# Kernel optimization log

Hardware: AMD Instinct MI355X
Metric: run time of the kernel (lower is better)

## Reference

```python
import jax, jax.numpy as jnp
import numpy as np

B, S, D, H, C = 8, 4096, 1024, 256, 512
INIT_RANGE = 0.01

def setup_inputs() -> dict:
    key = jax.random.key(0)
    ks = jax.random.split(key, 6)
    return {
        "hidden_states": jax.random.normal(ks[0], (B, S, D), dtype=jnp.float32),
        "conditions": jax.random.normal(ks[1], (B, C), dtype=jnp.float32),
        "down_project": jax.random.normal(ks[2], (D, H), dtype=jnp.float32) * INIT_RANGE,
        "down_gamma": jax.random.normal(ks[3], (C, H), dtype=jnp.float32),
        "down_beta": jnp.zeros((C, H), dtype=jnp.float32),
        "up_project": jax.random.normal(ks[4], (H, D), dtype=jnp.float32) * INIT_RANGE,
        "up_gamma": jax.random.normal(ks[5], (C, D), dtype=jnp.float32),
        "up_beta": jnp.zeros((C, D), dtype=jnp.float32),
    }

def reference(hidden_states, conditions, down_project, down_gamma, down_beta,
              up_project, up_gamma, up_beta):
    # per-example modulation coefficients: [B, H] / [B, D]
    dg = conditions @ down_gamma   # [B, H]
    db = conditions @ down_beta    # [B, H]
    ug = conditions @ up_gamma     # [B, D]
    ub = conditions @ up_beta      # [B, D]
    # per-example down weight: W_down * gamma (column scale) + beta (added to every row)
    w_down = down_project[None, :, :] * dg[:, None, :] + db[:, None, :]  # [B, D, H]
    down = jnp.einsum('bsd,bdh->bsh', hidden_states, w_down)             # [B, S, H]
    act = jax.nn.relu(down)
    w_up = up_project[None, :, :] * ug[:, None, :] + ub[:, None, :]      # [B, H, D]
    up = jnp.einsum('bsh,bhd->bsd', act, w_up)                           # [B, S, D]
    # (the original computes self.ln(up) but discards the result)
    return up + hidden_states
```

## Files before the change

kernel.cpp:

```cpp
#include <hip/hip_runtime.h>
#include <hip/hip_bf16.h>

typedef __attribute__((ext_vector_type(4))) float f32x4;
typedef __attribute__((ext_vector_type(8))) short s16x8;
typedef __attribute__((ext_vector_type(8))) unsigned short u16x8;
typedef __attribute__((ext_vector_type(4))) unsigned int u32x4;

#define DEVFN static __device__ __forceinline__

DEVFN unsigned short f2bf(float f) {
  union { float f; unsigned int u; } v; v.f = f;
  unsigned int u = v.u;
  u += 0x7fffu + ((u >> 16) & 1u);
  return (unsigned short)(u >> 16);
}

DEVFN unsigned int cvt_pk(float a, float b) {
  __hip_bfloat162 h = __float22bfloat162_rn(make_float2(a, b));
  union { __hip_bfloat162 h; unsigned int u; } v; v.h = h; return v.u;
}

DEVFN void gl_lds16(const void* g, void* l) {
  __builtin_amdgcn_global_load_lds((__attribute__((address_space(1))) void*)g,
                                   (__attribute__((address_space(3))) void*)l, 16, 0, 0);
}

#define DG_OFF 0
#define DB_OFF 2048
#define UG_OFF 4096
#define UB_OFF 12288
#define W1_BYTE 81920
#define W2_BYTE 606208

__global__ void prep_kernel(const float* __restrict__ cond,
                            const float* __restrict__ dgm, const float* __restrict__ dbt,
                            const float* __restrict__ ugm, const float* __restrict__ ubt,
                            const float* __restrict__ Wd, const float* __restrict__ Wu,
                            char* __restrict__ ws) {
  __shared__ float lc[4096];
  __shared__ float red[2048];
  const int t = threadIdx.x;

  if (blockIdx.x < 64) {
    const int bid = blockIdx.x;
    const float* src; char* dst; int C, ntile, kc;
    if (bid < 32) { src = Wd; C = 256;  ntile = bid >> 4; kc = bid & 15;
                    dst = ws + W1_BYTE + (size_t)(kc * 2 + ntile) * 16384; }
    else { int b2 = bid - 32; src = Wu; C = 1024; ntile = b2 >> 2; kc = b2 & 3;
           dst = ws + W2_BYTE + (size_t)(ntile * 4 + kc) * 16384; }
    const int n = t >> 1, kh = t & 1;
    const float* sp = src + (size_t)(kc * 64 + kh * 32) * C + ntile * 128 + n;
    unsigned short tmp[32];
#pragma unroll
    for (int kk = 0; kk < 32; ++kk) tmp[kk] = f2bf(sp[(size_t)kk * C]);
    char* drow = dst + n * 128;
#pragma unroll
    for (int gi = 0; gi < 4; ++gi) {
      u16x8 v;
#pragma unroll
      for (int e = 0; e < 8; ++e) v[e] = tmp[gi * 8 + e];
      int g = kh * 4 + gi;
      *(u16x8*)(drow + ((g ^ (n & 7)) << 4)) = v;
    }
    return;
  }

  float* coef = (float*)ws;
#pragma unroll
  for (int i = 0; i < 16; ++i) lc[t + i * 256] = cond[t + i * 256];
  __syncthreads();
  const int bid2 = blockIdx.x - 64;
  const int col = bid2 * 16 + (t & 15);
  const int ks = t >> 4;
  const float* src; int ncol, cl;
  if (col < 256)       { src = dgm; ncol = 256;  cl = col; }
  else if (col < 512)  { src = dbt; ncol = 256;  cl = col - 256; }
  else if (col < 1536) { src = ugm; ncol = 1024; cl = col - 512; }
  else                 { src = ubt; ncol = 1024; cl = col - 1536; }
  float acc[8] = {};
  for (int k = ks * 32; k < ks * 32 + 32; ++k) {
    float g = src[(size_t)k * ncol + cl];
#pragma unroll
    for (int b = 0; b < 8; ++b) acc[b] = fmaf(lc[b * 512 + k], g, acc[b]);
  }
#pragma unroll
  for (int b = 0; b < 8; ++b) red[(ks * 16 + (t & 15)) * 8 + b] = acc[b];
  __syncthreads();
  if (t < 128) {
    int c = t >> 3, b = t & 7;
    float s = 0.f;
#pragma unroll
    for (int k2 = 0; k2 < 16; ++k2) s += red[(k2 * 16 + c) * 8 + b];
    int colg = bid2 * 16 + c;
    float* dst; int ncol2, cl2;
    if (colg < 256)       { dst = coef + DG_OFF; ncol2 = 256;  cl2 = colg; }
    else if (colg < 512)  { dst = coef + DB_OFF; ncol2 = 256;  cl2 = colg - 256; }
    else if (colg < 1536) { dst = coef + UG_OFF; ncol2 = 1024; cl2 = colg - 512; }
    else                  { dst = coef + UB_OFF; ncol2 = 1024; cl2 = colg - 1536; }
    dst[b * ncol2 + cl2] = s;
  }
}

__global__ __launch_bounds__(512, 1)
void fused_kernel(const float* __restrict__ X, char* __restrict__ ws,
                  float* __restrict__ out) {
  __shared__ char lds[163840];
  const int tid = threadIdx.x;
  const int lane = tid & 63, wave = tid >> 6;
  const int lr = lane & 15, lq = lane >> 4;
  const int wm = wave >> 2, wn = wave & 3;

  const int m0 = blockIdx.x;
  const int row0 = m0 << 7;
  const int b = m0 >> 5;

  const float* coef = (const float*)ws;
  const char* w1 = ws + W1_BYTE;
  const char* w2 = ws + W2_BYTE;

  const int srow = tid >> 4, sg = tid & 15;
  const float* xsrc = X + (size_t)(row0 + srow) * 1024 + ((sg ^ (srow & 15)) << 2);

  int aoff[4][2][2], boff[4][2];
#pragma unroll
  for (int mf = 0; mf < 4; ++mf)
#pragma unroll
    for (int kf = 0; kf < 2; ++kf) {
      int r = wm * 64 + mf * 16 + lr;
      int g0 = kf * 8 + lq * 2;
      aoff[mf][kf][0] = r * 256 + ((g0 ^ (r & 15)) << 4);
      aoff[mf][kf][1] = r * 256 + (((g0 + 1) ^ (r & 15)) << 4);
    }
#pragma unroll
  for (int nf = 0; nf < 4; ++nf)
#pragma unroll
    for (int kf = 0; kf < 2; ++kf) {
      int n = wn * 64 + nf * 16 + lr;
      boff[nf][kf] = 131072 + (n >> 7) * 16384 + (n & 127) * 128 +
                     (((kf * 4 + lq) ^ (n & 7)) << 4);
    }

  f32x4 acc1[4][4] = {};
  float hacc[4] = {};

#define STAGE_X(t)                                                               \
  { char* xb = lds + 65536 + ((t) & 1) * 32768;                                  \
    _Pragma("unroll")                                                            \
    for (int i = 0; i < 4; ++i)                                                  \
      gl_lds16(xsrc + (size_t)((t) * 64) + (size_t)(i * 32) * 1024,              \
               xb + i * 8192 + tid * 16); }
#define STAGE_W1(t)                                                              \
  { _Pragma("unroll")                                                            \
    for (int i = 0; i < 4; ++i)                                                  \
      gl_lds16(w1 + (size_t)(t) * 32768 + i * 8192 + tid * 16,                   \
               lds + 131072 + i * 8192 + tid * 16); }

  STAGE_X(0); STAGE_X(1); STAGE_W1(0);
  asm volatile("s_waitcnt vmcnt(0)" ::: "memory");
  __builtin_amdgcn_sched_barrier(0);
  __builtin_amdgcn_s_barrier();
  __builtin_amdgcn_sched_barrier(0);

  for (int t = 0; t < 16; ++t) {
    const char* Xc = lds + 65536 + (t & 1) * 32768;
#pragma unroll
    for (int kf = 0; kf < 2; ++kf) {
      s16x8 afr[4], bfr[4];
#pragma unroll
      for (int mf = 0; mf < 4; ++mf) {
        f32x4 fa0 = *(const f32x4*)(Xc + aoff[mf][kf][0]);
        f32x4 fa1 = *(const f32x4*)(Xc + aoff[mf][kf][1]);
        if (wn == 0)
          hacc[mf] += fa0[0] + fa0[1] + fa0[2] + fa0[3] + fa1[0] + fa1[1] + fa1[2] + fa1[3];
        u32x4 p;
        p[0] = cvt_pk(fa0[0], fa0[1]); p[1] = cvt_pk(fa0[2], fa0[3]);
        p[2] = cvt_pk(fa1[0], fa1[1]); p[3] = cvt_pk(fa1[2], fa1[3]);
        union { u32x4 u; s16x8 s; } cv; cv.u = p; afr[mf] = cv.s;
      }
#pragma unroll
      for (int nf = 0; nf < 4; ++nf) bfr[nf] = *(const s16x8*)(lds + boff[nf][kf]);
#pragma unroll
      for (int mf = 0; mf < 4; ++mf)
#pragma unroll
        for (int nf = 0; nf < 4; ++nf)
          acc1[mf][nf] = __builtin_amdgcn_mfma_f32_16x16x32_bf16(afr[mf], bfr[nf], acc1[mf][nf], 0, 0, 0);
    }
    asm volatile("s_waitcnt lgkmcnt(0)" ::: "memory");
    __builtin_amdgcn_sched_barrier(0);
    __builtin_amdgcn_s_barrier();
    __builtin_amdgcn_sched_barrier(0);
    if (t < 15) {
      STAGE_W1(t + 1);
      if (t + 2 < 16) { STAGE_X(t + 2); asm volatile("s_waitcnt vmcnt(4)" ::: "memory"); }
      else            { asm volatile("s_waitcnt vmcnt(0)" ::: "memory"); }
      __builtin_amdgcn_sched_barrier(0);
      __builtin_amdgcn_s_barrier();
      __builtin_amdgcn_sched_barrier(0);
    }
  }

  float* hsumb = (float*)(lds + 65536);
  float* asp   = (float*)(lds + 65536 + 512);
  if (wn == 0) {
#pragma unroll
    for (int mf = 0; mf < 4; ++mf) {
      float s = hacc[mf];
      s += __shfl_xor(s, 16); s += __shfl_xor(s, 32);
      if (lq == 0) hsumb[wm * 64 + mf * 16 + lr] = s;
    }
  }
  __syncthreads();

  float dgv[4], dbv[4];
#pragma unroll
  for (int nf = 0; nf < 4; ++nf) {
    int h = wn * 64 + nf * 16 + lr;
    dgv[nf] = coef[DG_OFF + b * 256 + h];
    dbv[nf] = coef[DB_OFF + b * 256 + h];
  }

  float asacc[4][4] = {};
#pragma unroll
  for (int nf = 0; nf < 4; ++nf) {
    int g = nf * 2 + (lr >> 3);
    char* nbase = lds + wn * 16384 + (lr & 7) * 2;
    float dg_ = dgv[nf], db_ = dbv[nf];
#pragma unroll
    for (int mf = 0; mf < 4; ++mf) {
      int rb = wm * 64 + mf * 16 + lq * 4;
#pragma unroll
      for (int j = 0; j < 4; ++j) {
        int r = rb + j;
        float v = acc1[mf][nf][j] * dg_ + db_ * hsumb[r];
        v = fmaxf(v, 0.f);
        asacc[mf][j] += v;
        *(unsigned short*)(nbase + r * 128 + ((g ^ (r & 7)) << 4)) = f2bf(v);
      }
    }
  }
#pragma unroll
  for (int mf = 0; mf < 4; ++mf)
#pragma unroll
    for (int j = 0; j < 4; ++j) {
      float s = asacc[mf][j];
      s += __shfl_xor(s, 1); s += __shfl_xor(s, 2); s += __shfl_xor(s, 4); s += __shfl_xor(s, 8);
      if (lr == 0) asp[wn * 128 + wm * 64 + mf * 16 + lq * 4 + j] = s;
    }
  __syncthreads();

  float asv[4][4];
#pragma unroll
  for (int mf = 0; mf < 4; ++mf)
#pragma unroll
    for (int j = 0; j < 4; ++j) {
      int r = wm * 64 + mf * 16 + lq * 4 + j;
      asv[mf][j] = asp[r] + asp[128 + r] + asp[256 + r] + asp[384 + r];
    }
  float ugA[8][2], ubA[8][2];
#pragma unroll
  for (int nt = 0; nt < 8; ++nt)
#pragma unroll
    for (int nf = 0; nf < 2; ++nf) {
      int d = nt * 128 + wn * 32 + nf * 16 + lr;
      ugA[nt][nf] = coef[UG_OFF + b * 1024 + d];
      ubA[nt][nf] = coef[UB_OFF + b * 1024 + d];
    }

  int a2off[4][2], b2off[2][2];
#pragma unroll
  for (int mf = 0; mf < 4; ++mf)
#pragma unroll
    for (int kf = 0; kf < 2; ++kf) {
      int r = wm * 64 + mf * 16 + lr;
      a2off[mf][kf] = r * 128 + (((kf * 4 + lq) ^ (r & 7)) << 4);
    }
#pragma unroll
  for (int nf = 0; nf < 2; ++nf)
#pragma unroll
    for (int kf = 0; kf < 2; ++kf) {
      int nl = wn * 32 + nf * 16 + lr;
      b2off[nf][kf] = 131072 + nl * 128 + (((kf * 4 + lq) ^ (nl & 7)) << 4);
    }

#define STAGE_W2(s)                                                              \
  { _Pragma("unroll")                                                            \
    for (int i = 0; i < 2; ++i)                                                  \
      gl_lds16(w2 + (size_t)(s) * 16384 + i * 8192 + tid * 16,                   \
               lds + 131072 + ((s) & 1) * 16384 + i * 8192 + tid * 16); }

  STAGE_W2(0); STAGE_W2(1);
  asm volatile("s_waitcnt vmcnt(0)" ::: "memory");
  __builtin_amdgcn_sched_barrier(0);
  __builtin_amdgcn_s_barrier();
  __builtin_amdgcn_sched_barrier(0);

  f32x4 acc2[4][2];
  for (int s = 0; s < 32; ++s) {
    const int nt = s >> 2, kc = s & 3;
    if (kc == 0) {
#pragma unroll
      for (int mf = 0; mf < 4; ++mf)
#pragma unroll
        for (int nf = 0; nf < 2; ++nf) acc2[mf][nf] = (f32x4){0.f, 0.f, 0.f, 0.f};
    }
    const int bb = (s & 1) * 16384;
#pragma unroll
    for (int kf = 0; kf < 2; ++kf) {
      s16x8 afr[4], bfr[2];
#pragma unroll
      for (int mf = 0; mf < 4; ++mf)
        afr[mf] = *(const s16x8*)(lds + kc * 16384 + a2off[mf][kf]);
#pragma unroll
      for (int nf = 0; nf < 2; ++nf)
        bfr[nf] = *(const s16x8*)(lds + bb + b2off[nf][kf]);
#pragma unroll
      for (int mf = 0; mf < 4; ++mf)
#pragma unroll
        for (int nf = 0; nf < 2; ++nf)
          acc2[mf][nf] = __builtin_amdgcn_mfma_f32_16x16x32_bf16(afr[mf], bfr[nf], acc2[mf][nf], 0, 0, 0);
    }
    asm volatile("s_waitcnt lgkmcnt(0)" ::: "memory");
    __builtin_amdgcn_sched_barrier(0);
    __builtin_amdgcn_s_barrier();
    __builtin_amdgcn_sched_barrier(0);

    if (kc == 3) {
#pragma unroll
      for (int mf = 0; mf < 4; ++mf)
#pragma unroll
        for (int j = 0; j < 4; ++j) {
          int r = wm * 64 + mf * 16 + lq * 4 + j;
          size_t base = (size_t)(row0 + r) * 1024 + nt * 128;
          float as = asv[mf][j];
#pragma unroll
          for (int nf = 0; nf < 2; ++nf) {
            size_t gi = base + wn * 32 + nf * 16 + lr;
            out[gi] = acc2[mf][nf][j] * ugA[nt][nf] + ubA[nt][nf] * as + X[gi];
          }
        }
    }
    if (s + 2 < 32) STAGE_W2(s + 2);
    if (s < 31) {
      if (kc == 3 || s >= 30) asm volatile("s_waitcnt vmcnt(0)" ::: "memory");
      else                    asm volatile("s_waitcnt vmcnt(2)" ::: "memory");
      __builtin_amdgcn_sched_barrier(0);
      __builtin_amdgcn_s_barrier();
      __builtin_amdgcn_sched_barrier(0);
    }
  }
}

extern "C" void kernel_launch(void* const* d_in, const int* in_sizes, int n_in,
                              void* d_out, int out_size, void* d_ws, size_t ws_size,
                              hipStream_t stream) {
  const float* hidden       = (const float*)d_in[0];
  const float* conditions   = (const float*)d_in[1];
  const float* down_project = (const float*)d_in[2];
  const float* down_gamma   = (const float*)d_in[3];
  const float* down_beta    = (const float*)d_in[4];
  const float* up_project   = (const float*)d_in[5];
  const float* up_gamma     = (const float*)d_in[6];
  const float* up_beta      = (const float*)d_in[7];
  float* out = (float*)d_out;
  char* ws = (char*)d_ws;

  prep_kernel<<<224, 256, 0, stream>>>(conditions, down_gamma, down_beta, up_gamma, up_beta,
                                       down_project, up_project, ws);
  fused_kernel<<<256, 512, 0, stream>>>(hidden, ws, out);
}
```

Measured before the change: 96.72 us.

## Halve row tile to 64 rows, shrink LDS, and raise occupancy

```diff
diff --git a/kernel.cpp b/kernel.cpp
--- a/kernel.cpp
+++ b/kernel.cpp
@@ -24,6 +24,11 @@
   __builtin_amdgcn_global_load_lds((__attribute__((address_space(1))) void*)g,
                                    (__attribute__((address_space(3))) void*)l, 16, 0, 0);
 }
+
+#define SB() __builtin_amdgcn_sched_barrier(0)
+#define VMW(n) asm volatile("s_waitcnt vmcnt(" #n ")" ::: "memory")
+#define LGKM0() asm volatile("s_waitcnt lgkmcnt(0)" ::: "memory")
+#define BAR() { SB(); __builtin_amdgcn_s_barrier(); SB(); }
 
 #define DG_OFF 0
 #define DB_OFF 2048
@@ -41,26 +46,39 @@
   __shared__ float red[2048];
   const int t = threadIdx.x;
 
+  if (blockIdx.x < 32) {
+    const int ks = blockIdx.x;
+    const int n = t;
+    const float* sp = Wd + (size_t)(ks * 32) * 256 + n;
+    unsigned short tmp[32];
+#pragma unroll
+    for (int kk = 0; kk < 32; ++kk) tmp[kk] = f2bf(sp[(size_t)kk * 256]);
+    char* dst = ws + W1_BYTE + (size_t)ks * 16384 + n * 64;
+#pragma unroll
+    for (int g = 0; g < 4; ++g) {
+      u16x8 v;
+#pragma unroll
+      for (int e = 0; e < 8; ++e) v[e] = tmp[g * 8 + e];
+      *(u16x8*)(dst + ((g ^ ((n >> 1) & 3)) << 4)) = v;
+    }
+    return;
+  }
   if (blockIdx.x < 64) {
-    const int bid = blockIdx.x;
-    const float* src; char* dst; int C, ntile, kc;
-    if (bid < 32) { src = Wd; C = 256;  ntile = bid >> 4; kc = bid & 15;
-                    dst = ws + W1_BYTE + (size_t)(kc * 2 + ntile) * 16384; }
-    else { int b2 = bid - 32; src = Wu; C = 1024; ntile = b2 >> 2; kc = b2 & 3;
-           dst = ws + W2_BYTE + (size_t)(ntile * 4 + kc) * 16384; }
+    int b2 = blockIdx.x - 32;
+    int ntile = b2 >> 2, kc = b2 & 3;
     const int n = t >> 1, kh = t & 1;
-    const float* sp = src + (size_t)(kc * 64 + kh * 32) * C + ntile * 128 + n;
+    const float* sp = Wu + (size_t)(kc * 64 + kh * 32) * 1024 + ntile * 128 + n;
     unsigned short tmp[32];
 #pragma unroll
-    for (int kk = 0; kk < 32; ++kk) tmp[kk] = f2bf(sp[(size_t)kk * C]);
-    char* drow = dst + n * 128;
+    for (int kk = 0; kk < 32; ++kk) tmp[kk] = f2bf(sp[(size_t)kk * 1024]);
+    char* dst = ws + W2_BYTE + (size_t)(ntile * 4 + kc) * 16384 + n * 128;
 #pragma unroll
     for (int gi = 0; gi < 4; ++gi) {
       u16x8 v;
 #pragma unroll
       for (int e = 0; e < 8; ++e) v[e] = tmp[gi * 8 + e];
       int g = kh * 4 + gi;
-      *(u16x8*)(drow + ((g ^ (n & 7)) << 4)) = v;
+      *(u16x8*)(dst + ((g ^ (n & 7)) << 4)) = v;
     }
     return;
   }
@@ -101,18 +119,19 @@
   }
 }
 
-__global__ __launch_bounds__(512, 1)
+__global__ __launch_bounds__(512, 4)
 void fused_kernel(const float* __restrict__ X, char* __restrict__ ws,
                   float* __restrict__ out) {
-  __shared__ char lds[163840];
+  __shared__ char lds[81920];
   const int tid = threadIdx.x;
-  const int lane = tid & 63, wave = tid >> 6;
-  const int lr = lane & 15, lq = lane >> 4;
+  const int lane = tid & 63, lr = lane & 15, lq = lane >> 4;
+  const int wave = tid >> 6;
   const int wm = wave >> 2, wn = wave & 3;
 
-  const int m0 = blockIdx.x;
-  const int row0 = m0 << 7;
-  const int b = m0 >> 5;
+  const int raw = blockIdx.x;
+  const int m = (raw & 7) * 64 + (raw >> 3);
+  const int row0 = m << 6;
+  const int b = m >> 6;
 
   const float* coef = (const float*)ws;
   const char* w1 = ws + W1_BYTE;
@@ -121,92 +140,85 @@
   const int srow = tid >> 4, sg = tid & 15;
   const float* xsrc = X + (size_t)(row0 + srow) * 1024 + ((sg ^ (srow & 15)) << 2);
 
-  int aoff[4][2][2], boff[4][2];
-#pragma unroll
-  for (int mf = 0; mf < 4; ++mf)
-#pragma unroll
-    for (int kf = 0; kf < 2; ++kf) {
-      int r = wm * 64 + mf * 16 + lr;
-      int g0 = kf * 8 + lq * 2;
-      aoff[mf][kf][0] = r * 256 + ((g0 ^ (r & 15)) << 4);
-      aoff[mf][kf][1] = r * 256 + (((g0 + 1) ^ (r & 15)) << 4);
-    }
-#pragma unroll
-  for (int nf = 0; nf < 4; ++nf)
-#pragma unroll
-    for (int kf = 0; kf < 2; ++kf) {
-      int n = wn * 64 + nf * 16 + lr;
-      boff[nf][kf] = 131072 + (n >> 7) * 16384 + (n & 127) * 128 +
-                     (((kf * 4 + lq) ^ (n & 7)) << 4);
-    }
-
-  f32x4 acc1[4][4] = {};
-  float hacc[4] = {};
-
+  int aoff[2][2][2];
+#pragma unroll
+  for (int mf = 0; mf < 2; ++mf)
+#pragma unroll
+    for (int h = 0; h < 2; ++h) {
+      int r = wm * 32 + mf * 16 + lr;
+      int g0 = h * 8 + lq * 2;
+      aoff[mf][h][0] = r * 256 + ((g0 ^ (r & 15)) << 4);
+      aoff[mf][h][1] = r * 256 + (((g0 + 1) ^ (r & 15)) << 4);
+    }
+  int boff[4];
+#pragma unroll
+  for (int nf = 0; nf < 4; ++nf) {
+    int n = wn * 64 + nf * 16 + lr;
+    boff[nf] = n * 64 + ((lq ^ ((n >> 1) & 3)) << 4);
+  }
+
+  f32x4 acc1[2][4] = {};
+  float hacc[2] = {0.f, 0.f};
+
+#define XB(i) (lds + 32768 + (i) * 16384)
+#define W1B   (lds + 65536)
 #define STAGE_X(t)                                                               \
-  { char* xb = lds + 65536 + ((t) & 1) * 32768;                                  \
+  { char* xb = XB((t) & 1);                                                      \
+    gl_lds16(xsrc + (size_t)(t) * 64, xb + tid * 16);                            \
+    gl_lds16(xsrc + 32 * 1024 + (size_t)(t) * 64, xb + 8192 + tid * 16); }
+#define STAGE_W1(ks)                                                             \
+  { gl_lds16(w1 + (size_t)(ks) * 16384 + tid * 16, W1B + tid * 16);              \
+    gl_lds16(w1 + (size_t)(ks) * 16384 + 8192 + tid * 16, W1B + 8192 + tid * 16); }
+
+#define MFMA_SUB(Xc, h)                                                          \
+  { s16x8 afr[2];                                                                \
     _Pragma("unroll")                                                            \
-    for (int i = 0; i < 4; ++i)                                                  \
-      gl_lds16(xsrc + (size_t)((t) * 64) + (size_t)(i * 32) * 1024,              \
-               xb + i * 8192 + tid * 16); }
-#define STAGE_W1(t)                                                              \
-  { _Pragma("unroll")                                                            \
-    for (int i = 0; i < 4; ++i)                                                  \
-      gl_lds16(w1 + (size_t)(t) * 32768 + i * 8192 + tid * 16,                   \
-               lds + 131072 + i * 8192 + tid * 16); }
+    for (int mf = 0; mf < 2; ++mf) {                                             \
+      f32x4 fa0 = *(const f32x4*)((Xc) + aoff[mf][h][0]);                        \
+      f32x4 fa1 = *(const f32x4*)((Xc) + aoff[mf][h][1]);                        \
+      if (wn == 0)                                                               \
+        hacc[mf] += fa0[0] + fa0[1] + fa0[2] + fa0[3] +                          \
+                    fa1[0] + fa1[1] + fa1[2] + fa1[3];                           \
+      union { u32x4 u; s16x8 s; } cv;                                            \
+      cv.u[0] = cvt_pk(fa0[0], fa0[1]); cv.u[1] = cvt_pk(fa0[2], fa0[3]);        \
+      cv.u[2] = cvt_pk(fa1[0], fa1[1]); cv.u[3] = cvt_pk(fa1[2], fa1[3]);        \
+      afr[mf] = cv.s;                                                            \
+    }                                                                            \
+    s16x8 bfr[4];                                                                \
+    _Pragma("unroll")                                                            \
+    for (int nf = 0; nf < 4; ++nf) bfr[nf] = *(const s16x8*)(W1B + boff[nf]);    \
+    _Pragma("unroll")                                                            \
+    for (int mf = 0; mf < 2; ++mf)                                               \
+      _Pragma("unroll")                                                          \
+      for (int nf = 0; nf < 4; ++nf)                                             \
+        acc1[mf][nf] = __builtin_amdgcn_mfma_f32_16x16x32_bf16(afr[mf], bfr[nf], \
+                                                               acc1[mf][nf], 0, 0, 0); }
 
   STAGE_X(0); STAGE_X(1); STAGE_W1(0);
-  asm volatile("s_waitcnt vmcnt(0)" ::: "memory");
-  __builtin_amdgcn_sched_barrier(0);
-  __builtin_amdgcn_s_barrier();
-  __builtin_amdgcn_sched_barrier(0);
+  VMW(0); BAR();
 
   for (int t = 0; t < 16; ++t) {
-    const char* Xc = lds + 65536 + (t & 1) * 32768;
-#pragma unroll
-    for (int kf = 0; kf < 2; ++kf) {
-      s16x8 afr[4], bfr[4];
-#pragma unroll
-      for (int mf = 0; mf < 4; ++mf) {
-        f32x4 fa0 = *(const f32x4*)(Xc + aoff[mf][kf][0]);
-        f32x4 fa1 = *(const f32x4*)(Xc + aoff[mf][kf][1]);
-        if (wn == 0)
-          hacc[mf] += fa0[0] + fa0[1] + fa0[2] + fa0[3] + fa1[0] + fa1[1] + fa1[2] + fa1[3];
-        u32x4 p;
-        p[0] = cvt_pk(fa0[0], fa0[1]); p[1] = cvt_pk(fa0[2], fa0[3]);
-        p[2] = cvt_pk(fa1[0], fa1[1]); p[3] = cvt_pk(fa1[2], fa1[3]);
-        union { u32x4 u; s16x8 s; } cv; cv.u = p; afr[mf] = cv.s;
-      }
-#pragma unroll
-      for (int nf = 0; nf < 4; ++nf) bfr[nf] = *(const s16x8*)(lds + boff[nf][kf]);
-#pragma unroll
-      for (int mf = 0; mf < 4; ++mf)
-#pragma unroll
-        for (int nf = 0; nf < 4; ++nf)
-          acc1[mf][nf] = __builtin_amdgcn_mfma_f32_16x16x32_bf16(afr[mf], bfr[nf], acc1[mf][nf], 0, 0, 0);
-    }
-    asm volatile("s_waitcnt lgkmcnt(0)" ::: "memory");
-    __builtin_amdgcn_sched_barrier(0);
-    __builtin_amdgcn_s_barrier();
-    __builtin_amdgcn_sched_barrier(0);
-    if (t < 15) {
-      STAGE_W1(t + 1);
-      if (t + 2 < 16) { STAGE_X(t + 2); asm volatile("s_waitcnt vmcnt(4)" ::: "memory"); }
-      else            { asm volatile("s_waitcnt vmcnt(0)" ::: "memory"); }
-      __builtin_amdgcn_sched_barrier(0);
-      __builtin_amdgcn_s_barrier();
-      __builtin_amdgcn_sched_barrier(0);
-    }
-  }
-
-  float* hsumb = (float*)(lds + 65536);
-  float* asp   = (float*)(lds + 65536 + 512);
+    const char* Xc = XB(t & 1);
+    MFMA_SUB(Xc, 0);
+    LGKM0(); BAR();
+    STAGE_W1(2 * t + 1);
+    VMW(0); BAR();
+    MFMA_SUB(Xc, 1);
+    LGKM0(); BAR();
+    if (t < 15) STAGE_W1(2 * t + 2);
+    if (t < 14) { STAGE_X(t + 2); VMW(2); }
+    else        { VMW(0); }
+    BAR();
+  }
+
+  float* hsumb = (float*)(lds + 32768);
+  float* asp   = (float*)(lds + 33024);
   if (wn == 0) {
 #pragma unroll
-    for (int mf = 0; mf < 4; ++mf) {
+    for (int mf = 0; mf < 2; ++mf) {
       float s = hacc[mf];
       s += __shfl_xor(s, 16); s += __shfl_xor(s, 32);
-      if (lq == 0) hsumb[wm * 64 + mf * 16 + lr] = s;
+      if (lq == 0) hsumb[wm * 32 + mf * 16 + lr] = s;
     }
   }
   __syncthreads();
@@ -219,18 +231,17 @@
     dbv[nf] = coef[DB_OFF + b * 256 + h];
   }
 
-  float asacc[4][4] = {};
+  float asacc[2][4] = {};
 #pragma unroll
   for (int nf = 0; nf < 4; ++nf) {
     int g = nf * 2 + (lr >> 3);
-    char* nbase = lds + wn * 16384 + (lr & 7) * 2;
+    char* nbase = lds + wn * 8192 + (lr & 7) * 2;
     float dg_ = dgv[nf], db_ = dbv[nf];
 #pragma unroll
-    for (int mf = 0; mf < 4; ++mf) {
-      int rb = wm * 64 + mf * 16 + lq * 4;
+    for (int mf = 0; mf < 2; ++mf) {
 #pragma unroll
       for (int j = 0; j < 4; ++j) {
-        int r = rb + j;
+        int r = wm * 32 + mf * 16 + lq * 4 + j;
         float v = acc1[mf][nf][j] * dg_ + db_ * hsumb[r];
         v = fmaxf(v, 0.f);
         asacc[mf][j] += v;
@@ -239,39 +250,31 @@
     }
   }
 #pragma unroll
-  for (int mf = 0; mf < 4; ++mf)
+  for (int mf = 0; mf < 2; ++mf)
 #pragma unroll
     for (int j = 0; j < 4; ++j) {
       float s = asacc[mf][j];
       s += __shfl_xor(s, 1); s += __shfl_xor(s, 2); s += __shfl_xor(s, 4); s += __shfl_xor(s, 8);
-      if (lr == 0) asp[wn * 128 + wm * 64 + mf * 16 + lq * 4 + j] = s;
-    }
-  __syncthreads();
-
-  float asv[4][4];
-#pragma unroll
-  for (int mf = 0; mf < 4; ++mf)
+      if (lr == 0) asp[wn * 64 + wm * 32 + mf * 16 + lq * 4 + j] = s;
+    }
+  __syncthreads();
+
+  float asv[2][4];
+#pragma unroll
+  for (int mf = 0; mf < 2; ++mf)
 #pragma unroll
     for (int j = 0; j < 4; ++j) {
-      int r = wm * 64 + mf * 16 + lq * 4 + j;
-      asv[mf][j] = asp[r] + asp[128 + r] + asp[256 + r] + asp[384 + r];
-    }
-  float ugA[8][2], ubA[8][2];
-#pragma unroll
-  for (int nt = 0; nt < 8; ++nt)
-#pragma unroll
-    for (int nf = 0; nf < 2; ++nf) {
-      int d = nt * 128 + wn * 32 + nf * 16 + lr;
-      ugA[nt][nf] = coef[UG_OFF + b * 1024 + d];
-      ubA[nt][nf] = coef[UB_OFF + b * 1024 + d];
-    }
-
-  int a2off[4][2], b2off[2][2];
-#pragma unroll
-  for (int mf = 0; mf < 4; ++mf)
+      int r = wm * 32 + mf * 16 + lq * 4 + j;
+      asv[mf][j] = asp[r] + asp[64 + r] + asp[128 + r] + asp[192 + r];
+    }
+  __syncthreads();
+
+  int a2off[2][2], b2off[2][2];
+#pragma unroll
+  for (int mf = 0; mf < 2; ++mf)
 #pragma unroll
     for (int kf = 0; kf < 2; ++kf) {
-      int r = wm * 64 + mf * 16 + lr;
+      int r = wm * 32 + mf * 16 + lr;
       a2off[mf][kf] = r * 128 + (((kf * 4 + lq) ^ (r & 7)) << 4);
     }
 #pragma unroll
@@ -279,74 +282,78 @@
 #pragma unroll
     for (int kf = 0; kf < 2; ++kf) {
       int nl = wn * 32 + nf * 16 + lr;
-      b2off[nf][kf] = 131072 + nl * 128 + (((kf * 4 + lq) ^ (nl & 7)) << 4);
-    }
-
+      b2off[nf][kf] = nl * 128 + (((kf * 4 + lq) ^ (nl & 7)) << 4);
+    }
+
+#define W2B(s) (lds + 32768 + ((s) % 3) * 16384)
 #define STAGE_W2(s)                                                              \
-  { _Pragma("unroll")                                                            \
-    for (int i = 0; i < 2; ++i)                                                  \
-      gl_lds16(w2 + (size_t)(s) * 16384 + i * 8192 + tid * 16,                   \
-               lds + 131072 + ((s) & 1) * 16384 + i * 8192 + tid * 16); }
+  { gl_lds16(w2 + (size_t)(s) * 16384 + tid * 16, W2B(s) + tid * 16);            \
+    gl_lds16(w2 + (size_t)(s) * 16384 + 8192 + tid * 16,                         \
+             W2B(s) + 8192 + tid * 16); }
 
   STAGE_W2(0); STAGE_W2(1);
-  asm volatile("s_waitcnt vmcnt(0)" ::: "memory");
-  __builtin_amdgcn_sched_barrier(0);
-  __builtin_amdgcn_s_barrier();
-  __builtin_amdgcn_sched_barrier(0);
-
-  f32x4 acc2[4][2];
+  VMW(2); BAR();
+
+  float ugv[2], ubv[2];
+#pragma unroll
   for (int s = 0; s < 32; ++s) {
     const int nt = s >> 2, kc = s & 3;
+    f32x4 acc2[2][2];
     if (kc == 0) {
 #pragma unroll
-      for (int mf = 0; mf < 4; ++mf)
+      for (int mf = 0; mf < 2; ++mf)
 #pragma unroll
         for (int nf = 0; nf < 2; ++nf) acc2[mf][nf] = (f32x4){0.f, 0.f, 0.f, 0.f};
     }
-    const int bb = (s & 1) * 16384;
+    static f32x4 dummy;
+    const char* Wb = W2B(s);
 #pragma unroll
     for (int kf = 0; kf < 2; ++kf) {
-      s16x8 afr[4], bfr[2];
-#pragma unroll
-      for (int mf = 0; mf < 4; ++mf)
-        afr[mf] = *(const s16x8*)(lds + kc * 16384 + a2off[mf][kf]);
+      s16x8 a2[2], bb[2];
+#pragma unroll
+      for (int mf = 0; mf < 2; ++mf)
+        a2[mf] = *(const s16x8*)(lds + kc * 8192 + a2off[mf][kf]);
 #pragma unroll
       for (int nf = 0; nf < 2; ++nf)
-        bfr[nf] = *(const s16x8*)(lds + bb + b2off[nf][kf]);
-#pragma unroll
-      for (int mf = 0; mf < 4; ++mf)
+        bb[nf] = *(const s16x8*)(Wb + b2off[nf][kf]);
+#pragma unroll
+      for (int mf = 0; mf < 2; ++mf)
 #pragma unroll
         for (int nf = 0; nf < 2; ++nf)
-          acc2[mf][nf] = __builtin_amdgcn_mfma_f32_16x16x32_bf16(afr[mf], bfr[nf], acc2[mf][nf], 0, 0, 0);
-    }
-    asm volatile("s_waitcnt lgkmcnt(0)" ::: "memory");
-    __builtin_amdgcn_sched_barrier(0);
-    __builtin_amdgcn_s_barrier();
-    __builtin_amdgcn_sched_barrier(0);
-
+          acc2[mf][nf] = __builtin_amdgcn_mfma_f32_16x16x32_bf16(a2[mf], bb[nf], acc2[mf][nf], 0, 0, 0);
+    }
+    LGKM0(); BAR();
+
+    if (kc == 0) {
+#pragma unroll
+      for (int nf = 0; nf < 2; ++nf) {
+        int d = nt * 128 + wn * 32 + nf * 16 + lr;
+        ugv[nf] = coef[UG_OFF + b * 1024 + d];
+        ubv[nf] = coef[UB_OFF + b * 1024 + d];
+      }
+    }
+    if (s + 2 < 32) STAGE_W2(s + 2);
     if (kc == 3) {
 #pragma unroll
-      for (int mf = 0; mf < 4; ++mf)
+      for (int mf = 0; mf < 2; ++mf)
 #pragma unroll
         for (int j = 0; j < 4; ++j) {
-          int r = wm * 64 + mf * 16 + lq * 4 + j;
-          size_t base = (size_t)(row0 + r) * 1024 + nt * 128;
-          float as = asv[mf][j];
+          int r = wm * 32 + mf * 16 + lq * 4 + j;
+          size_t gbase = (size_t)(row0 + r) * 1024 + nt * 128 + wn * 32;
 #pragma unroll
           for (int nf = 0; nf < 2; ++nf) {
-            size_t gi = base + wn * 32 + nf * 16 + lr;
-            out[gi] = acc2[mf][nf][j] * ugA[nt][nf] + ubA[nt][nf] * as + X[gi];
+            size_t gi = gbase + nf * 16 + lr;
+            out[gi] = acc2[mf][nf][j] * ugv[nf] + ubv[nf] * asv[mf][j] + X[gi];
           }
         }
     }
-    if (s + 2 < 32) STAGE_W2(s + 2);
     if (s < 31) {
-      if (kc == 3 || s >= 30) asm volatile("s_waitcnt vmcnt(0)" ::: "memory");
-      else                    asm volatile("s_waitcnt vmcnt(2)" ::: "memory");
-      __builtin_amdgcn_sched_barrier(0);
-      __builtin_amdgcn_s_barrier();
-      __builtin_amdgcn_sched_barrier(0);
-    }
+      if (s + 2 >= 32)  { VMW(0); }
+      else if (kc == 3) { VMW(16); }
+      else              { VMW(2); }
+      BAR();
+    }
+    (void)dummy;
   }
 }
 
@@ -366,5 +373,5 @@
 
   prep_kernel<<<224, 256, 0, stream>>>(conditions, down_gamma, down_beta, up_gamma, up_beta,
                                        down_project, up_project, ws);
-  fused_kernel<<<256, 512, 0, stream>>>(hidden, ws, out);
-}
+  fused_kernel<<<512, 512, 0, stream>>>(hidden, ws, out);
+}
```

Result: faster. 89.42 us (-7.6%).
